# Performance work log

Measured on AMD Instinct MI355X. Metric: run time of the kernel, lower is better.

## Reference

```python
import jax, jax.numpy as jnp
import numpy as np
import math

MIN_NORM = 1e-15
EPS = 1e-7
MAX_NORM = 1e6

N = 100000      # num nodes (aaa)
E = 1600000     # num edges
D_IN = 129      # embedding_num (1 time coord + 128 spatial)
D_OUT = 128     # output1_dim
MAXLEN = 50
B = 4096
NCLASS = 5

# ---------------- Hyperboloid manifold ops (HGCN-style) ----------------

def proj(x, c):
    K = 1. / c
    y = x[..., 1:]
    y_sq = jnp.sum(y * y, axis=-1, keepdims=True)
    x0 = jnp.sqrt(jnp.clip(K + y_sq, EPS))
    return jnp.concatenate([x0, y], axis=-1)

def proj_tan0(u, c):
    # zero out the time coordinate
    return jnp.concatenate([jnp.zeros_like(u[..., :1]), u[..., 1:]], axis=-1)

def expmap0(u, c):
    K = 1. / c
    sqrtK = jnp.sqrt(K)
    x = u[..., 1:]
    xn = jnp.maximum(jnp.linalg.norm(x, axis=-1, keepdims=True), MIN_NORM)
    theta = xn / sqrtK
    first = sqrtK * jnp.cosh(theta)
    rest = sqrtK * jnp.sinh(theta) * x / xn
    return proj(jnp.concatenate([first, rest], axis=-1), c)

def logmap0(x, c):
    K = 1. / c
    sqrtK = jnp.sqrt(K)
    y = x[..., 1:]
    yn = jnp.maximum(jnp.linalg.norm(y, axis=-1, keepdims=True), MIN_NORM)
    theta = jnp.clip(x[..., 0:1] / sqrtK, 1.0 + EPS)
    rest = sqrtK * jnp.arccosh(theta) * y / yn
    return jnp.concatenate([jnp.zeros_like(theta), rest], axis=-1)

def minkowski_dot(x, y):
    return jnp.sum(x * y, axis=-1, keepdims=True) - 2.0 * x[..., 0:1] * y[..., 0:1]

def minkowski_norm(u):
    return jnp.sqrt(jnp.clip(minkowski_dot(u, u), EPS))

def expmap(u, x, c):
    K = 1. / c
    sqrtK = jnp.sqrt(K)
    normu = jnp.minimum(minkowski_norm(u), MAX_NORM)
    theta = jnp.maximum(normu / sqrtK, MIN_NORM)
    result = jnp.cosh(theta) * x + jnp.sinh(theta) * u / theta
    return proj(result, c)

def proj_tan(u, x, c):
    ux = jnp.sum(x[..., 1:] * u[..., 1:], axis=-1, keepdims=True)
    vals0 = ux / jnp.clip(x[..., 0:1], EPS)
    return jnp.concatenate([vals0, u[..., 1:]], axis=-1)

def ptransp0(x, u, c):
    K = 1. / c
    sqrtK = jnp.sqrt(K)
    x0 = x[..., 0:1]
    y = x[..., 1:]
    yn = jnp.maximum(jnp.linalg.norm(y, axis=-1, keepdims=True), MIN_NORM)
    yhat = y / yn
    v = jnp.concatenate([-yn, (sqrtK - x0) * yhat], axis=-1)
    alpha = jnp.sum(yhat * u[..., 1:], axis=-1, keepdims=True) / sqrtK
    return proj_tan(u - alpha * v, x, c)

def mobius_add(x, y, c):
    u = logmap0(y, c)
    v = ptransp0(x, jnp.broadcast_to(u, x.shape), c)
    return expmap(v, x, c)

def mobius_add0(x, y, c):
    # tangent-space addition at the origin
    return expmap0(logmap0(x, c) + logmap0(y, c), c)

def mobius_matvec1(m, x, c):
    return expmap0(logmap0(x, c) @ m, c)

def mobius_matvec0(n, x, c):
    # per-row scalar mobius scaling (n is (N,1))
    return expmap0(n * logmap0(x, c), c)

def hyp_bias_point(b, c):
    return proj(expmap0(proj_tan0(b[None, :], c), c), c)

def gcn_layer(x, w, b, rows, cols, vals, c, n_nodes):
    out = mobius_matvec1(w, x, c)
    out = mobius_add(out, hyp_bias_point(b, c), c)
    out = logmap0(out, c)
    out = jax.ops.segment_sum(vals[:, None] * out[cols], rows, num_segments=n_nodes)
    return proj(expmap0(out, c), c)


def setup_inputs() -> dict:
    key = jax.random.key(0)
    ks = jax.random.split(key, 20)
    def ku(k, shape, fan_in):
        bound = 1.0 / math.sqrt(fan_in)
        return jax.random.uniform(k, shape, jnp.float32, -bound, bound)
    inp = {}
    inp['A1_tensor'] = jax.random.normal(ks[0], (N, D_IN), jnp.float32)
    inp['adj_rows'] = jax.random.randint(ks[1], (E,), 0, N)
    inp['adj_cols'] = jax.random.randint(ks[2], (E,), 0, N)
    inp['adj_vals'] = jax.random.uniform(ks[3], (E,), jnp.float32) * 0.1
    inp['batch_idx'] = jax.random.randint(ks[4], (B, 1, MAXLEN), 0, N)
    inp['raw_c'] = jnp.array([math.log(math.exp(1.0) - 1.0)], jnp.float32)
    inp['n_param'] = jax.random.uniform(ks[5], (N, 1), jnp.float32)
    inp['Lin1'] = ku(ks[6], (D_IN, D_OUT), D_IN)
    inp['Lin1_bias'] = ku(ks[7], (D_OUT,), D_IN)
    inp['gc1_w'] = ku(ks[8], (D_IN, D_OUT), D_IN)
    inp['gc1_b'] = ku(ks[9], (D_OUT,), D_IN)
    inp['gc2_w'] = ku(ks[10], (D_OUT, D_OUT), D_OUT)
    inp['gc2_b'] = ku(ks[11], (D_OUT,), D_OUT)
    inp['weight'] = ku(ks[12], (D_OUT, MAXLEN), D_OUT)
    inp['weight2'] = ku(ks[13], (D_OUT, MAXLEN), D_OUT)
    inp['conv1_w'] = ku(ks[14], (MAXLEN,), MAXLEN)
    inp['conv1_b'] = ku(ks[15], (1,), MAXLEN)
    inp['conv2_w'] = ku(ks[16], (MAXLEN,), MAXLEN)
    inp['conv2_b'] = ku(ks[17], (1,), MAXLEN)
    inp['classifier'] = ku(ks[18], (2 * MAXLEN, NCLASS), 2 * MAXLEN)
    inp['classifier_bias'] = ku(ks[19], (NCLASS,), 2 * MAXLEN)
    return inp


def reference(A1_tensor, adj_rows, adj_cols, adj_vals, batch_idx, raw_c, n_param,
              Lin1, Lin1_bias, gc1_w, gc1_b, gc2_w, gc2_b, weight, weight2,
              conv1_w, conv1_b, conv2_w, conv2_b, classifier, classifier_bias):
    c = jax.nn.softplus(raw_c)[0] + 1e-5
    bi = batch_idx[:, 0, :]                       # (B, L)
    flat = bi.reshape(-1)

    x_tan = proj_tan0(A1_tensor, c)
    a = proj(expmap0(x_tan, c), c)                # (N, D_IN)

    a1 = mobius_matvec1(Lin1, a, c)               # (N, D_OUT)
    a1 = mobius_add(a1, hyp_bias_point(Lin1_bias, c), c)
    a2 = mobius_matvec0(n_param, a1, c)

    x_1 = gcn_layer(a, gc1_w, gc1_b, adj_rows, adj_cols, adj_vals, c, N)
    x_1 = mobius_matvec0(1.0 - n_param, x_1, c)
    x_1 = mobius_add0(x_1, a2, c)
    x_2 = gcn_layer(x_1, gc2_w, gc2_b, adj_rows, adj_cols, adj_vals, c, N)

    # readout branch 1: x_2 gathered on batch indices
    s2 = logmap0(x_2[flat].reshape(bi.shape[0], bi.shape[1], D_OUT), c)  # (B,L,D)
    s2 = jnp.einsum('bld,dt->blt', s2, weight)    # (B, L, MAXLEN)
    s2 = jnp.einsum('blt,l->bt', s2, conv1_w) + conv1_b  # kernel-size-1 conv over channels

    # readout branch 2: a1 gathered on batch indices
    s3 = logmap0(a1[flat].reshape(bi.shape[0], bi.shape[1], D_OUT), c)
    s3 = jnp.einsum('bld,dt->blt', s3, weight2)
    s3 = jnp.einsum('blt,l->bt', s3, conv2_w) + conv2_b

    sel = jnp.concatenate([s2, s3], axis=1)       # (B, 2*MAXLEN)
    pre = sel @ classifier + classifier_bias      # (B, NCLASS)
    return jnp.argmax(pre, axis=-1), sel
```

## Files before the change

### kernel.cpp

```cpp
#include <hip/hip_runtime.h>
#include <math.h>


typedef unsigned short ushort_t;
typedef __attribute__((ext_vector_type(8))) short short8;
typedef __attribute__((ext_vector_type(4))) float f32x4;

__device__ __forceinline__ float wsum(float x){
  x += __shfl_xor(x, 32);
  x += __shfl_xor(x, 16);
  x += __shfl_xor(x, 8);
  x += __shfl_xor(x, 4);
  x += __shfl_xor(x, 2);
  x += __shfl_xor(x, 1);
  return x;
}

__device__ __forceinline__ void get_c(const float* rc, float& K, float& sK){
  float c = log1pf(expf(rc[0])) + 1e-5f;
  K  = 1.0f / c;
  sK = sqrtf(K);
}

__device__ __forceinline__ float sinhx_over_x(float x){
  if (x > 1e-3f){
    float e  = __expf(x);
    float em = __builtin_amdgcn_rcpf(e);
    return 0.5f*(e - em) * __builtin_amdgcn_rcpf(x);
  }
  return 1.0f + x*x*(1.0f/6.0f);
}

__device__ __forceinline__ float facosh(float x){
  return __logf(x + sqrtf(fmaxf(fmaf(x, x, -1.0f), 0.0f)));
}

__device__ __forceinline__ ushort_t bf16_rne(float x){
  unsigned int u = __float_as_uint(x);
  u += 0x7fffu + ((u >> 16) & 1u);
  return (ushort_t)(u >> 16);
}
__device__ __forceinline__ float bf2f(ushort_t h){
  return __uint_as_float(((unsigned int)h) << 16);
}
__device__ __forceinline__ unsigned int pack_bf16(float x, float y){
  unsigned int bx = __float_as_uint(x);
  unsigned int by = __float_as_uint(y);
  bx = (bx + 0x7fffu + ((bx >> 16) & 1u)) >> 16;
  by = (by + 0x7fffu + ((by >> 16) & 1u)) & 0xffff0000u;
  return bx | by;
}
__device__ __forceinline__ float bf_lo(unsigned int p){ return __uint_as_float(p << 16); }
__device__ __forceinline__ float bf_hi(unsigned int p){ return __uint_as_float(p & 0xffff0000u); }

__device__ __forceinline__ void chain_scalars(float tt, float tu, float uu,
                                              float K, float sK,
                                              float& At, float& Au){
  float xn  = fmaxf(sqrtf(tt), 1e-15f);
  float th  = xn / sK;
  float f   = sinhx_over_x(th);
  float pn2 = f*f*tt;
  float p0  = sqrtf(fmaxf(K + pn2, 1e-7f));
  float S_yu = f * tu;
  float yn  = fmaxf(sqrtf(pn2), 1e-15f);
  float inv_yn = __builtin_amdgcn_rcpf(yn);
  float alpha = S_yu * inv_yn / sK;
  float coef  = alpha * (sK - p0);
  float cy  = coef * inv_yn;
  float cyf = cy * f;
  float pdw  = S_yu - cy*pn2;
  float spsq = uu - 2.f*cy*S_yu + cy*cy*pn2;
  float w0 = pdw / fmaxf(p0, 1e-7f);
  float md = spsq - w0*w0;
  float normu = fminf(sqrtf(fmaxf(md, 1e-7f)), 1e6f);
  float th2 = fmaxf(normu / sK, 1e-15f);
  float e  = __expf(th2);
  float em = __builtin_amdgcn_rcpf(e);
  float ch = 0.5f*(e + em);
  float g  = (th2 > 1e-3f) ? 0.5f*(e - em)*__builtin_amdgcn_rcpf(th2)
                           : 1.0f + th2*th2*(1.0f/6.0f);
  float rn2 = ch*ch*pn2 + 2.f*ch*g*pdw + g*g*spsq;
  float r0 = sqrtf(fmaxf(K + rn2, 1e-7f));
  float ynf = fmaxf(sqrtf(rn2), 1e-15f);
  float thf = fmaxf(r0/sK, 1.f+1e-7f);
  float rf = sK * facosh(thf) * __builtin_amdgcn_rcpf(ynf);
  At = rf*(ch*f - g*cyf);
  Au = rf*g;
}

__global__ __launch_bounds__(256) void stage_a(const float* __restrict__ A1,
                                               ushort_t* __restrict__ Lhi,
                                               ushort_t* __restrict__ Llo,
                                               int* __restrict__ cnt,
                                               const float* __restrict__ b0,
                                               const float* __restrict__ b1,
                                               const float* __restrict__ b2,
                                               float* __restrict__ uu3, int n){
  size_t i = (size_t)blockIdx.x * 256 + threadIdx.x;
  size_t total = (size_t)n * 128;
  if (i < total){
    size_t row = i >> 7; int j = (int)(i & 127);
    float v = A1[row*129 + 1 + j];
    ushort_t h = bf16_rne(v);
    Lhi[i] = h;
    Llo[i] = bf16_rne(v - bf2f(h));
  }
  if (i < (size_t)n) cnt[i] = 0;
  if (blockIdx.x == 0 && threadIdx.x < 64){
    int lane = threadIdx.x;
    const float* bs[3] = {b0, b1, b2};
    for (int k = 0; k < 3; ++k){
      float x = lane ? bs[k][2*lane] : 0.0f;
      float y = bs[k][2*lane+1];
      float s = wsum(x*x + y*y);
      if (lane == 0) uu3[k] = s;
    }
  }
}

__global__ __launch_bounds__(256) void split_w(const float* __restrict__ W,
                                               ushort_t* __restrict__ Whi,
                                               ushort_t* __restrict__ Wlo){
  int id = blockIdx.x * 256 + threadIdx.x;
  int k = id >> 7, nn = id & 127;
  float v = W[(size_t)k*128 + nn];
  ushort_t h = bf16_rne(v);
  Whi[(size_t)nn*128 + k] = h;
  Wlo[(size_t)nn*128 + k] = bf16_rne(v - bf2f(h));
}

__global__ __launch_bounds__(256) void mfma_chain(const ushort_t* __restrict__ Ahi,
                                                  const ushort_t* __restrict__ Alo,
                                                  const ushort_t* __restrict__ Whi,
                                                  const ushort_t* __restrict__ Wlo,
                                                  const float* __restrict__ bias,
                                                  const float* __restrict__ uu3, int uuidx,
                                                  const float* __restrict__ raw_c,
                                                  float* __restrict__ outF,
                                                  unsigned int* __restrict__ outH,
                                                  int mode, int n, int nWaves){
  __shared__ ushort_t Wsh[2][128*128];
  int tid = threadIdx.x;
  {
    const uint4* gh = (const uint4*)Whi;
    const uint4* gl = (const uint4*)Wlo;
    uint4* sh = (uint4*)Wsh[0];
    uint4* sl = (uint4*)Wsh[1];
    #pragma unroll
    for (int i = 0; i < 8; ++i){ sh[tid + 256*i] = gh[tid + 256*i]; }
    #pragma unroll
    for (int i = 0; i < 8; ++i){ sl[tid + 256*i] = gl[tid + 256*i]; }
  }
  __syncthreads();

  int lane = tid & 63;
  int c = lane & 15, quad = lane >> 4;
  int wid = blockIdx.x * 4 + (tid >> 6);
  int nStrips = (n + 15) >> 4;

  float K, sK; get_c(raw_c, K, sK);
  float uu = uu3[uuidx];
  float uv[8];
  #pragma unroll
  for (int t = 0; t < 8; ++t){
    int col = t*16 + c;
    uv[t] = (col == 0) ? 0.f : bias[col];
  }

  for (int strip = wid; strip < nStrips; strip += nWaves){
    int m0 = strip * 16;
    int ra = m0 + c; if (ra > n - 1) ra = n - 1;
    short8 ahi[4], alo[4];
    #pragma unroll
    for (int kc = 0; kc < 4; ++kc){
      size_t aoff = (size_t)ra*128 + kc*32 + quad*8;
      ahi[kc] = *(const short8*)&Ahi[aoff];
      alo[kc] = *(const short8*)&Alo[aoff];
    }

    f32x4 acc[8];
    #pragma unroll
    for (int t = 0; t < 8; ++t){
      f32x4 z = {0.f, 0.f, 0.f, 0.f};
      acc[t] = z;
      int wrow = (t*16 + c) * 128;
      #pragma unroll
      for (int kc = 0; kc < 4; ++kc){
        int woff = wrow + kc*32 + quad*8;
        short8 bhi = *(const short8*)&Wsh[0][woff];
        short8 blo = *(const short8*)&Wsh[1][woff];
        acc[t] = __builtin_amdgcn_mfma_f32_16x16x32_bf16(ahi[kc], bhi, acc[t], 0, 0, 0);
        acc[t] = __builtin_amdgcn_mfma_f32_16x16x32_bf16(ahi[kc], blo, acc[t], 0, 0, 0);
        acc[t] = __builtin_amdgcn_mfma_f32_16x16x32_bf16(alo[kc], bhi, acc[t], 0, 0, 0);
      }
    }

    if (c == 0){
      f32x4 z = {0.f, 0.f, 0.f, 0.f};
      acc[0] = z;
    }
    #pragma unroll
    for (int r = 0; r < 4; ++r){
      float tt = 0.f, tu = 0.f;
      #pragma unroll
      for (int t = 0; t < 8; ++t){
        float v = acc[t][r];
        tt = fmaf(v, v, tt);
        tu = fmaf(v, uv[t], tu);
      }
      #pragma unroll
      for (int m = 1; m <= 8; m <<= 1){
        tt += __shfl_xor(tt, m);
        tu += __shfl_xor(tu, m);
      }
      float At, Au; chain_scalars(tt, tu, uu, K, sK, At, Au);
      int row = m0 + quad*4 + r;
      if (mode == 0){
        if (row < n){
          #pragma unroll
          for (int t = 0; t < 8; ++t){
            float o = fmaf(At, acc[t][r], Au*uv[t]);
            outF[(size_t)row*128 + t*16 + c] = o;
          }
        }
      } else {
        #pragma unroll
        for (int t = 0; t < 8; ++t){
          float o  = fmaf(At, acc[t][r], Au*uv[t]);
          float on = __shfl_xor(o, 1);
          if (row < n && !(c & 1))
            outH[(size_t)row*64 + t*8 + (c >> 1)] = pack_bf16(o, on);
        }
      }
    }
  }
}

__global__ __launch_bounds__(256) void hist_k(const int* __restrict__ rows,
                                              int* __restrict__ cnt,
                                              int* __restrict__ rnk, int e){
  int base = (blockIdx.x * 256 + threadIdx.x) * 4;
  if (base + 3 < e){
    int4 r = *(const int4*)&rows[base];
    int k0 = atomicAdd(&cnt[r.x], 1);
    int k1 = atomicAdd(&cnt[r.y], 1);
    int k2 = atomicAdd(&cnt[r.z], 1);
    int k3 = atomicAdd(&cnt[r.w], 1);
    *(int4*)&rnk[base] = make_int4(k0, k1, k2, k3);
  } else {
    for (int i = base; i < e; ++i) rnk[i] = atomicAdd(&cnt[rows[i]], 1);
  }
}

#define SCAN_ITEMS 4
__global__ __launch_bounds__(256) void scan1(const int* __restrict__ cnt,
                                             int* __restrict__ off,
                                             int* __restrict__ bsum, int n){
  __shared__ int sh[256];
  int tid = threadIdx.x;
  int base = blockIdx.x * 256 * SCAN_ITEMS + tid * SCAN_ITEMS;
  int v[SCAN_ITEMS]; int s = 0;
  #pragma unroll
  for (int i = 0; i < SCAN_ITEMS; ++i){ int idx = base+i; v[i] = (idx < n) ? cnt[idx] : 0; s += v[i]; }
  sh[tid] = s; __syncthreads();
  for (int o = 1; o < 256; o <<= 1){
    int t = (tid >= o) ? sh[tid - o] : 0; __syncthreads();
    sh[tid] += t; __syncthreads();
  }
  int excl = sh[tid] - s;
  if (tid == 255) bsum[blockIdx.x] = sh[tid];
  int run = excl;
  #pragma unroll
  for (int i = 0; i < SCAN_ITEMS; ++i){ int idx = base+i; if (idx < n) off[idx] = run; run += v[i]; }
}

__global__ void scan2(int* bsum, int G){
  if (threadIdx.x == 0 && blockIdx.x == 0){
    int run = 0;
    for (int i = 0; i < G; ++i){ int t = bsum[i]; bsum[i] = run; run += t; }
  }
}

__global__ void scan3(int* __restrict__ off, const int* __restrict__ bsum, int n){
  int i = blockIdx.x * blockDim.x + threadIdx.x;
  if (i < n) off[i] += bsum[i / (256*SCAN_ITEMS)];
}

__global__ __launch_bounds__(256) void fill_k(const int* __restrict__ rows,
                                              const int* __restrict__ cols,
                                              const float* __restrict__ vals,
                                              const int* __restrict__ off,
                                              const int* __restrict__ rnk,
                                              int2* __restrict__ ecv, int e){
  int base = (blockIdx.x * 256 + threadIdx.x) * 4;
  if (base + 3 < e){
    int4   r = *(const int4*)&rows[base];
    int4   q = *(const int4*)&rnk[base];
    int4   c = *(const int4*)&cols[base];
    float4 v = *(const float4*)&vals[base];
    int o0 = off[r.x], o1 = off[r.y], o2 = off[r.z], o3 = off[r.w];
    ecv[o0 + q.x] = make_int2(c.x, __float_as_int(v.x));
    ecv[o1 + q.y] = make_int2(c.y, __float_as_int(v.y));
    ecv[o2 + q.z] = make_int2(c.z, __float_as_int(v.z));
    ecv[o3 + q.w] = make_int2(c.w, __float_as_int(v.w));
  } else {
    for (int i = base; i < e; ++i)
      ecv[off[rows[i]] + rnk[i]] = make_int2(cols[i], __float_as_int(vals[i]));
  }
}

__device__ __forceinline__ float2 seg_gather_bf16(const unsigned int* __restrict__ h,
                                                  const int* __restrict__ off,
                                                  const int* __restrict__ cnt,
                                                  const int2* __restrict__ ecv,
                                                  int row, int lane){
  float ax = 0.f, ay = 0.f, bx = 0.f, by = 0.f;
  int st = off[row], deg = cnt[row];
  const unsigned int* __restrict__ hb = h + lane;
  for (int b = 0; b < deg; b += 64){
    int k = b + lane;
    int cc = 0; float vv = 0.f;
    if (k < deg){ int2 e = ecv[st+k]; cc = e.x; vv = __int_as_float(e.y); }
    int m = min(64, deg - b);
    for (int j = 0; j < m; j += 8){
      int   c0=__shfl(cc,j+0), c1=__shfl(cc,j+1), c2=__shfl(cc,j+2), c3=__shfl(cc,j+3);
      int   c4=__shfl(cc,j+4), c5=__shfl(cc,j+5), c6=__shfl(cc,j+6), c7=__shfl(cc,j+7);
      float v0=__shfl(vv,j+0), v1=__shfl(vv,j+1), v2=__shfl(vv,j+2), v3=__shfl(vv,j+3);
      float v4=__shfl(vv,j+4), v5=__shfl(vv,j+5), v6=__shfl(vv,j+6), v7=__shfl(vv,j+7);
      unsigned int p0 = hb[(size_t)c0*64];
      unsigned int p1 = hb[(size_t)c1*64];
      unsigned int p2 = hb[(size_t)c2*64];
      unsigned int p3 = hb[(size_t)c3*64];
      unsigned int p4 = hb[(size_t)c4*64];
      unsigned int p5 = hb[(size_t)c5*64];
      unsigned int p6 = hb[(size_t)c6*64];
      unsigned int p7 = hb[(size_t)c7*64];
      ax = fmaf(v0, bf_lo(p0), ax); ay = fmaf(v0, bf_hi(p0), ay);
      bx = fmaf(v1, bf_lo(p1), bx); by = fmaf(v1, bf_hi(p1), by);
      ax = fmaf(v2, bf_lo(p2), ax); ay = fmaf(v2, bf_hi(p2), ay);
      bx = fmaf(v3, bf_lo(p3), bx); by = fmaf(v3, bf_hi(p3), by);
      ax = fmaf(v4, bf_lo(p4), ax); ay = fmaf(v4, bf_hi(p4), ay);
      bx = fmaf(v5, bf_lo(p5), bx); by = fmaf(v5, bf_hi(p5), by);
      ax = fmaf(v6, bf_lo(p6), ax); ay = fmaf(v6, bf_hi(p6), ay);
      bx = fmaf(v7, bf_lo(p7), bx); by = fmaf(v7, bf_hi(p7), by);
    }
  }
  return make_float2(ax + bx, ay + by);
}

__global__ __launch_bounds__(256) void seg_x1(const unsigned int* __restrict__ h1,
                                              const int* __restrict__ off,
                                              const int* __restrict__ cnt,
                                              const int2* __restrict__ ecv,
                                              const float* __restrict__ loga1,
                                              const float* __restrict__ nparam,
                                              unsigned int* __restrict__ X1hi,
                                              unsigned int* __restrict__ X1lo, int n){
  int row  = (int)((blockIdx.x * blockDim.x + threadIdx.x) >> 6);
  int lane = threadIdx.x & 63;
  if (row >= n) return;
  float2 acc = seg_gather_bf16(h1, off, cnt, ecv, row, lane);
  float nv = nparam[row];
  float2 la1 = *(const float2*)&loga1[(size_t)row*128 + 2*lane];
  float ox = (1.f-nv)*acc.x + nv*la1.x;
  float oy = (1.f-nv)*acc.y + nv*la1.y;
  unsigned int hp = pack_bf16(ox, oy);
  X1hi[(size_t)row*64 + lane] = hp;
  X1lo[(size_t)row*64 + lane] = pack_bf16(ox - bf_lo(hp), oy - bf_hi(hp));
}

__global__ __launch_bounds__(256) void seg_x2(const unsigned int* __restrict__ h2,
                                              const int* __restrict__ off,
                                              const int* __restrict__ cnt,
                                              const int2* __restrict__ ecv,
                                              float* __restrict__ Lx2, int n){
  int row  = (int)((blockIdx.x * blockDim.x + threadIdx.x) >> 6);
  int lane = threadIdx.x & 63;
  if (row >= n) return;
  float2 acc = seg_gather_bf16(h2, off, cnt, ecv, row, lane);
  *(float2*)&Lx2[(size_t)row*128 + 2*lane] = acc;
}

__global__ __launch_bounds__(128) void batch_head(const float* __restrict__ Lx2,
                                                  const float* __restrict__ loga1,
                                                  const int* __restrict__ bidx,
                                                  const float* __restrict__ weight,
                                                  const float* __restrict__ weight2,
                                                  const float* __restrict__ c1w,
                                                  const float* __restrict__ c1b,
                                                  const float* __restrict__ c2w,
                                                  const float* __restrict__ c2b,
                                                  const float* __restrict__ cls,
                                                  const float* __restrict__ clsb,
                                                  float* __restrict__ out, int Bn){
  __shared__ float sg2[128], sg3[128], ssel[100], spre[5];
  __shared__ int sbi[50];
  __shared__ float sc1[50], sc2[50];
  int b = blockIdx.x, d = threadIdx.x;
  const int* bi = bidx + (size_t)b * 50;
  if (d < 50){ sbi[d] = bi[d]; sc1[d] = c1w[d]; sc2[d] = c2w[d]; }
  __syncthreads();
  int lane = d & 63;
  bool lo = d < 64;
  const float* __restrict__ tab = lo ? Lx2 : loga1;
  const float* __restrict__ cw = lo ? sc1 : sc2;
  float gx = 0.f, gy = 0.f;
  const float2* __restrict__ t2 = (const float2*)tab + lane;
  #pragma unroll
  for (int l = 0; l < 50; l += 5){
    int i0 = sbi[l+0], i1 = sbi[l+1], i2 = sbi[l+2], i3 = sbi[l+3], i4 = sbi[l+4];
    float2 p0 = t2[(size_t)i0*64];
    float2 p1 = t2[(size_t)i1*64];
    float2 p2 = t2[(size_t)i2*64];
    float2 p3 = t2[(size_t)i3*64];
    float2 p4 = t2[(size_t)i4*64];
    float w0 = cw[l+0], w1 = cw[l+1], w2 = cw[l+2], w3 = cw[l+3], w4 = cw[l+4];
    gx = fmaf(w0, p0.x, gx); gy = fmaf(w0, p0.y, gy);
    gx = fmaf(w1, p1.x, gx); gy = fmaf(w1, p1.y, gy);
    gx = fmaf(w2, p2.x, gx); gy = fmaf(w2, p2.y, gy);
    gx = fmaf(w3, p3.x, gx); gy = fmaf(w3, p3.y, gy);
    gx = fmaf(w4, p4.x, gx); gy = fmaf(w4, p4.y, gy);
  }
  if (lo){ sg2[2*lane] = gx; sg2[2*lane+1] = gy; }
  else   { sg3[2*lane] = gx; sg3[2*lane+1] = gy; }
  __syncthreads();
  if (d < 50){
    float s = 0.f;
    for (int k = 0; k < 128; ++k) s = fmaf(sg2[k], weight[k*50 + d], s);
    s += c1b[0];
    ssel[d] = s;
    out[(size_t)Bn + (size_t)b*100 + d] = s;
  } else if (d >= 64 && d < 114){
    int t = d - 64;
    float s = 0.f;
    for (int k = 0; k < 128; ++k) s = fmaf(sg3[k], weight2[k*50 + t], s);
    s += c2b[0];
    ssel[50 + t] = s;
    out[(size_t)Bn + (size_t)b*100 + 50 + t] = s;
  }
  __syncthreads();
  if (d < 5){
    float s = clsb[d];
    for (int j = 0; j < 100; ++j) s = fmaf(ssel[j], cls[j*5 + d], s);
    spre[d] = s;
  }
  __syncthreads();
  if (d == 0){
    int best = 0; float bv = spre[0];
    #pragma unroll
    for (int k = 1; k < 5; ++k) if (spre[k] > bv){ bv = spre[k]; best = k; }
    out[b] = (float)best;
  }
}

extern "C" void kernel_launch(void* const* d_in, const int* in_sizes, int n_in,
                              void* d_out, int out_size, void* d_ws, size_t ws_size,
                              hipStream_t stream) {
  const float* A1     = (const float*)d_in[0];
  const int*   rows   = (const int*)  d_in[1];
  const int*   cols   = (const int*)  d_in[2];
  const float* vals   = (const float*)d_in[3];
  const int*   bidx   = (const int*)  d_in[4];
  const float* raw_c  = (const float*)d_in[5];
  const float* nparam = (const float*)d_in[6];
  const float* Lin1   = (const float*)d_in[7];
  const float* Lin1_b = (const float*)d_in[8];
  const float* gc1_w  = (const float*)d_in[9];
  const float* gc1_b  = (const float*)d_in[10];
  const float* gc2_w  = (const float*)d_in[11];
  const float* gc2_b  = (const float*)d_in[12];
  const float* weight = (const float*)d_in[13];
  const float* weight2= (const float*)d_in[14];
  const float* c1w    = (const float*)d_in[15];
  const float* c1b    = (const float*)d_in[16];
  const float* c2w    = (const float*)d_in[17];
  const float* c2b    = (const float*)d_in[18];
  const float* cls    = (const float*)d_in[19];
  const float* clsb   = (const float*)d_in[20];

  int N  = in_sizes[0] / 129;
  int E  = in_sizes[1];
  int Bn = in_sizes[4] / 50;
  size_t NF = (size_t)N * 128;

  ushort_t* Lhi = (ushort_t*)d_ws;
  ushort_t* Llo = Lhi + NF;
  float*    S0  = (float*)d_ws;
  float*    S3  = (float*)(Llo + NF);
  unsigned int* Hb   = (unsigned int*)(S3 + NF);
  unsigned int* X1hi = Hb + NF/2;
  unsigned int* X1lo = X1hi + NF/2;
  ushort_t* Wb = (ushort_t*)(X1lo + NF/2);
  ushort_t* W1h = Wb,           *W1l = Wb + 16384;
  ushort_t* W2h = Wb + 2*16384, *W2l = Wb + 3*16384;
  ushort_t* W3h = Wb + 4*16384, *W3l = Wb + 5*16384;
  int* cnt    = (int*)(Wb + 6*16384);
  int* off    = cnt + N;
  int* rnk    = off + N;
  int* bsum   = rnk + E;
  int2* ecv   = (int2*)(bsum + 4096);
  float* uu3  = (float*)(ecv + E);

  int rowBlocks  = (N + 3) / 4;
  int G = (N + 256*SCAN_ITEMS - 1) / (256*SCAN_ITEMS);
  int eBlocks4 = (E/4 + 255) / 256 + 1;
  int mBlocks = 512;
  int nWaves  = mBlocks * 4;

  stage_a<<<(int)((NF + 255)/256), 256, 0, stream>>>(A1, Lhi, Llo, cnt,
                                                     Lin1_b, gc1_b, gc2_b, uu3, N);
  split_w<<<64, 256, 0, stream>>>(Lin1 + 128, W1h, W1l);
  split_w<<<64, 256, 0, stream>>>(gc1_w + 128, W2h, W2l);
  split_w<<<64, 256, 0, stream>>>(gc2_w, W3h, W3l);

  hist_k<<<eBlocks4, 256, 0, stream>>>(rows, cnt, rnk, E);
  scan1<<<G, 256, 0, stream>>>(cnt, off, bsum, N);
  scan2<<<1, 64, 0, stream>>>(bsum, G);
  scan3<<<(N+255)/256, 256, 0, stream>>>(off, bsum, N);
  fill_k<<<eBlocks4, 256, 0, stream>>>(rows, cols, vals, off, rnk, ecv, E);

  mfma_chain<<<mBlocks, 256, 0, stream>>>(Lhi, Llo, W1h, W1l, Lin1_b, uu3, 0, raw_c,
                                          S3, (unsigned int*)nullptr, 0, N, nWaves);
  mfma_chain<<<mBlocks, 256, 0, stream>>>(Lhi, Llo, W2h, W2l, gc1_b, uu3, 1, raw_c,
                                          (float*)nullptr, Hb, 1, N, nWaves);
  seg_x1<<<rowBlocks, 256, 0, stream>>>(Hb, off, cnt, ecv, S3, nparam, X1hi, X1lo, N);
  mfma_chain<<<mBlocks, 256, 0, stream>>>((const ushort_t*)X1hi, (const ushort_t*)X1lo,
                                          W3h, W3l, gc2_b, uu3, 2, raw_c,
                                          (float*)nullptr, Hb, 1, N, nWaves);
  seg_x2<<<rowBlocks, 256, 0, stream>>>(Hb, off, cnt, ecv, S0, N);
  batch_head<<<Bn, 128, 0, stream>>>(S0, S3, bidx, weight, weight2, c1w, c1b,
                                     c2w, c2b, cls, clsb, (float*)d_out, Bn);
}
```

Before: 625.5 us.

## Overlap CSR build and readout branch with MFMA GEMMs via auxiliary warps

The edge histogram, CSR fill, and the a1 readout branch move into extra warps of the mfma_chain launches, so this latency-bound scatter and gather work overlaps the GEMM passes. Those launches grow from 256 to 320 or 384 threads. The change also vectorizes stage_a, merges the three split_w launches into one, parallelizes scan2, and stores the second GCN output as bf16 so the final head gathers half the bytes. The risks are extra register and scheduling pressure on the GEMM blocks, and a small loss of precision in the x_2 readout.

```diff
diff --git a/kernel.cpp b/kernel.cpp
--- a/kernel.cpp
+++ b/kernel.cpp
@@ -5,6 +5,7 @@
 typedef unsigned short ushort_t;
 typedef __attribute__((ext_vector_type(8))) short short8;
 typedef __attribute__((ext_vector_type(4))) float f32x4;
+typedef __attribute__((ext_vector_type(4))) unsigned short u16x4;
 
 __device__ __forceinline__ float wsum(float x){
   x += __shfl_xor(x, 32);
@@ -96,16 +97,20 @@
                                                const float* __restrict__ b1,
                                                const float* __restrict__ b2,
                                                float* __restrict__ uu3, int n){
-  size_t i = (size_t)blockIdx.x * 256 + threadIdx.x;
-  size_t total = (size_t)n * 128;
-  if (i < total){
-    size_t row = i >> 7; int j = (int)(i & 127);
-    float v = A1[row*129 + 1 + j];
-    ushort_t h = bf16_rne(v);
-    Lhi[i] = h;
-    Llo[i] = bf16_rne(v - bf2f(h));
-  }
-  if (i < (size_t)n) cnt[i] = 0;
+  size_t i4 = (size_t)blockIdx.x * 256 + threadIdx.x;
+  size_t tot4 = (size_t)n * 32;
+  if (i4 < tot4){
+    size_t row = i4 >> 5; int j0 = (int)(i4 & 31) * 4;
+    const float* s = A1 + row*129 + 1 + j0;
+    float v0 = s[0], v1 = s[1], v2 = s[2], v3 = s[3];
+    ushort_t h0 = bf16_rne(v0), h1 = bf16_rne(v1), h2 = bf16_rne(v2), h3 = bf16_rne(v3);
+    u16x4 hh = {h0, h1, h2, h3};
+    u16x4 ll = {bf16_rne(v0 - bf2f(h0)), bf16_rne(v1 - bf2f(h1)),
+                bf16_rne(v2 - bf2f(h2)), bf16_rne(v3 - bf2f(h3))};
+    *(u16x4*)&Lhi[i4*4] = hh;
+    *(u16x4*)&Llo[i4*4] = ll;
+  }
+  if (i4 < (size_t)n) cnt[i4] = 0;
   if (blockIdx.x == 0 && threadIdx.x < 64){
     int lane = threadIdx.x;
     const float* bs[3] = {b0, b1, b2};
@@ -118,10 +123,16 @@
   }
 }
 
-__global__ __launch_bounds__(256) void split_w(const float* __restrict__ W,
-                                               ushort_t* __restrict__ Whi,
-                                               ushort_t* __restrict__ Wlo){
-  int id = blockIdx.x * 256 + threadIdx.x;
+__global__ __launch_bounds__(256) void split_w3(const float* __restrict__ Lin1,
+                                                const float* __restrict__ G1,
+                                                const float* __restrict__ G2,
+                                                ushort_t* __restrict__ Wb){
+  int bid = blockIdx.x;
+  int which = bid >> 6, b = bid & 63;
+  const float* W = (which == 0) ? (Lin1 + 128) : (which == 1) ? (G1 + 128) : G2;
+  ushort_t* Whi = Wb + (size_t)which * 2 * 16384;
+  ushort_t* Wlo = Whi + 16384;
+  int id = b * 256 + threadIdx.x;
   int k = id >> 7, nn = id & 127;
   float v = W[(size_t)k*128 + nn];
   ushort_t h = bf16_rne(v);
@@ -129,7 +140,7 @@
   Wlo[(size_t)nn*128 + k] = bf16_rne(v - bf2f(h));
 }
 
-__global__ __launch_bounds__(256) void mfma_chain(const ushort_t* __restrict__ Ahi,
+__global__ __launch_bounds__(384) void mfma_chain(const ushort_t* __restrict__ Ahi,
                                                   const ushort_t* __restrict__ Alo,
                                                   const ushort_t* __restrict__ Whi,
                                                   const ushort_t* __restrict__ Wlo,
@@ -138,10 +149,25 @@
                                                   const float* __restrict__ raw_c,
                                                   float* __restrict__ outF,
                                                   unsigned int* __restrict__ outH,
-                                                  int mode, int n, int nWaves){
+                                                  int mode, int n, int nWaves,
+                                                  int aux, int epb, int e,
+                                                  const int* __restrict__ erows,
+                                                  const int* __restrict__ ecols,
+                                                  const float* __restrict__ evals,
+                                                  int* __restrict__ cnt,
+                                                  int* __restrict__ rnk,
+                                                  const int* __restrict__ off,
+                                                  int2* __restrict__ ecv,
+                                                  const float* __restrict__ loga1,
+                                                  const int* __restrict__ bidx,
+                                                  const float* __restrict__ c2w,
+                                                  const float* __restrict__ c2b,
+                                                  const float* __restrict__ weight2,
+                                                  float* __restrict__ sel3,
+                                                  float* __restrict__ outTop, int Bn){
   __shared__ ushort_t Wsh[2][128*128];
   int tid = threadIdx.x;
-  {
+  if (tid < 256){
     const uint4* gh = (const uint4*)Whi;
     const uint4* gl = (const uint4*)Wlo;
     uint4* sh = (uint4*)Wsh[0];
@@ -154,8 +180,91 @@
   __syncthreads();
 
   int lane = tid & 63;
+  int warp = tid >> 6;
+
+  if (warp >= 4){
+    if (aux == 1){
+      int gpl = epb >> 8;
+      int gbase = (blockIdx.x * epb) >> 2;
+      for (int k = 0; k < gpl; ++k){
+        int b4 = (gbase + k*64 + lane) * 4;
+        if (b4 + 3 < e){
+          int4 r = *(const int4*)&erows[b4];
+          int k0 = atomicAdd(&cnt[r.x], 1);
+          int k1 = atomicAdd(&cnt[r.y], 1);
+          int k2 = atomicAdd(&cnt[r.z], 1);
+          int k3 = atomicAdd(&cnt[r.w], 1);
+          *(int4*)&rnk[b4] = make_int4(k0, k1, k2, k3);
+        } else {
+          for (int i = b4; i < e; ++i) rnk[i] = atomicAdd(&cnt[erows[i]], 1);
+        }
+      }
+    } else if (aux == 2){
+      int gpl = epb >> 8;
+      int gbase = (blockIdx.x * epb) >> 2;
+      for (int k = 0; k < gpl; ++k){
+        int b4 = (gbase + k*64 + lane) * 4;
+        if (b4 + 3 < e){
+          int4   r = *(const int4*)&erows[b4];
+          int4   q = *(const int4*)&rnk[b4];
+          int4   cc = *(const int4*)&ecols[b4];
+          float4 vv = *(const float4*)&evals[b4];
+          int o0 = off[r.x], o1 = off[r.y], o2 = off[r.z], o3 = off[r.w];
+          ecv[o0 + q.x] = make_int2(cc.x, __float_as_int(vv.x));
+          ecv[o1 + q.y] = make_int2(cc.y, __float_as_int(vv.y));
+          ecv[o2 + q.z] = make_int2(cc.z, __float_as_int(vv.z));
+          ecv[o3 + q.w] = make_int2(cc.w, __float_as_int(vv.w));
+        } else {
+          for (int i = b4; i < e; ++i)
+            ecv[off[erows[i]] + rnk[i]] = make_int2(ecols[i], __float_as_int(evals[i]));
+        }
+      }
+    } else if (aux == 3){
+      float cw = (lane < 50) ? c2w[lane] : 0.f;
+      for (int q = 0; q < 4; ++q){
+        int b = blockIdx.x * 8 + (warp - 4) * 4 + q;
+        if (b >= Bn) break;
+        int bi = (lane < 50) ? bidx[(size_t)b*50 + lane] : 0;
+        float gx = 0.f, gy = 0.f;
+        #pragma unroll
+        for (int l = 0; l < 50; l += 5){
+          int i0 = __shfl(bi, l+0), i1 = __shfl(bi, l+1), i2 = __shfl(bi, l+2);
+          int i3 = __shfl(bi, l+3), i4 = __shfl(bi, l+4);
+          float w0 = __shfl(cw, l+0), w1 = __shfl(cw, l+1), w2v = __shfl(cw, l+2);
+          float w3 = __shfl(cw, l+3), w4 = __shfl(cw, l+4);
+          float2 p0 = *(const float2*)&loga1[(size_t)i0*128 + 2*lane];
+          float2 p1 = *(const float2*)&loga1[(size_t)i1*128 + 2*lane];
+          float2 p2 = *(const float2*)&loga1[(size_t)i2*128 + 2*lane];
+          float2 p3 = *(const float2*)&loga1[(size_t)i3*128 + 2*lane];
+          float2 p4 = *(const float2*)&loga1[(size_t)i4*128 + 2*lane];
+          gx = fmaf(w0, p0.x, gx); gy = fmaf(w0, p0.y, gy);
+          gx = fmaf(w1, p1.x, gx); gy = fmaf(w1, p1.y, gy);
+          gx = fmaf(w2v, p2.x, gx); gy = fmaf(w2v, p2.y, gy);
+          gx = fmaf(w3, p3.x, gx); gy = fmaf(w3, p3.y, gy);
+          gx = fmaf(w4, p4.x, gx); gy = fmaf(w4, p4.y, gy);
+        }
+        float s = 0.f;
+        #pragma unroll 8
+        for (int d = 0; d < 128; d += 2){
+          float ge = __shfl(gx, d >> 1);
+          float go = __shfl(gy, d >> 1);
+          if (lane < 50){
+            s = fmaf(ge, weight2[d*50 + lane], s);
+            s = fmaf(go, weight2[(d+1)*50 + lane], s);
+          }
+        }
+        if (lane < 50){
+          float v = s + c2b[0];
+          sel3[(size_t)b*50 + lane] = v;
+          outTop[(size_t)Bn + (size_t)b*100 + 50 + lane] = v;
+        }
+      }
+    }
+    return;
+  }
+
   int c = lane & 15, quad = lane >> 4;
-  int wid = blockIdx.x * 4 + (tid >> 6);
+  int wid = blockIdx.x * 4 + warp;
   int nStrips = (n + 15) >> 4;
 
   float K, sK; get_c(raw_c, K, sK);
@@ -236,22 +345,6 @@
   }
 }
 
-__global__ __launch_bounds__(256) void hist_k(const int* __restrict__ rows,
-                                              int* __restrict__ cnt,
-                                              int* __restrict__ rnk, int e){
-  int base = (blockIdx.x * 256 + threadIdx.x) * 4;
-  if (base + 3 < e){
-    int4 r = *(const int4*)&rows[base];
-    int k0 = atomicAdd(&cnt[r.x], 1);
-    int k1 = atomicAdd(&cnt[r.y], 1);
-    int k2 = atomicAdd(&cnt[r.z], 1);
-    int k3 = atomicAdd(&cnt[r.w], 1);
-    *(int4*)&rnk[base] = make_int4(k0, k1, k2, k3);
-  } else {
-    for (int i = base; i < e; ++i) rnk[i] = atomicAdd(&cnt[rows[i]], 1);
-  }
-}
-
 #define SCAN_ITEMS 4
 __global__ __launch_bounds__(256) void scan1(const int* __restrict__ cnt,
                                              int* __restrict__ off,
@@ -274,39 +367,21 @@
   for (int i = 0; i < SCAN_ITEMS; ++i){ int idx = base+i; if (idx < n) off[idx] = run; run += v[i]; }
 }
 
-__global__ void scan2(int* bsum, int G){
-  if (threadIdx.x == 0 && blockIdx.x == 0){
-    int run = 0;
-    for (int i = 0; i < G; ++i){ int t = bsum[i]; bsum[i] = run; run += t; }
-  }
+__global__ __launch_bounds__(256) void scan2(int* __restrict__ bsum, int G){
+  __shared__ int sh[256];
+  int t = threadIdx.x;
+  int v = (t < G) ? bsum[t] : 0;
+  sh[t] = v; __syncthreads();
+  for (int o = 1; o < 256; o <<= 1){
+    int x = (t >= o) ? sh[t - o] : 0; __syncthreads();
+    sh[t] += x; __syncthreads();
+  }
+  if (t < G) bsum[t] = sh[t] - v;
 }
 
 __global__ void scan3(int* __restrict__ off, const int* __restrict__ bsum, int n){
   int i = blockIdx.x * blockDim.x + threadIdx.x;
   if (i < n) off[i] += bsum[i / (256*SCAN_ITEMS)];
-}
-
-__global__ __launch_bounds__(256) void fill_k(const int* __restrict__ rows,
-                                              const int* __restrict__ cols,
-                                              const float* __restrict__ vals,
-                                              const int* __restrict__ off,
-                                              const int* __restrict__ rnk,
-                                              int2* __restrict__ ecv, int e){
-  int base = (blockIdx.x * 256 + threadIdx.x) * 4;
-  if (base + 3 < e){
-    int4   r = *(const int4*)&rows[base];
-    int4   q = *(const int4*)&rnk[base];
-    int4   c = *(const int4*)&cols[base];
-    float4 v = *(const float4*)&vals[base];
-    int o0 = off[r.x], o1 = off[r.y], o2 = off[r.z], o3 = off[r.w];
-    ecv[o0 + q.x] = make_int2(c.x, __float_as_int(v.x));
-    ecv[o1 + q.y] = make_int2(c.y, __float_as_int(v.y));
-    ecv[o2 + q.z] = make_int2(c.z, __float_as_int(v.z));
-    ecv[o3 + q.w] = make_int2(c.w, __float_as_int(v.w));
-  } else {
-    for (int i = base; i < e; ++i)
-      ecv[off[rows[i]] + rnk[i]] = make_int2(cols[i], __float_as_int(vals[i]));
-  }
 }
 
 __device__ __forceinline__ float2 seg_gather_bf16(const unsigned int* __restrict__ h,
@@ -373,79 +448,71 @@
                                               const int* __restrict__ off,
                                               const int* __restrict__ cnt,
                                               const int2* __restrict__ ecv,
-                                              float* __restrict__ Lx2, int n){
+                                              unsigned int* __restrict__ Lx2p, int n){
   int row  = (int)((blockIdx.x * blockDim.x + threadIdx.x) >> 6);
   int lane = threadIdx.x & 63;
   if (row >= n) return;
   float2 acc = seg_gather_bf16(h2, off, cnt, ecv, row, lane);
-  *(float2*)&Lx2[(size_t)row*128 + 2*lane] = acc;
-}
-
-__global__ __launch_bounds__(128) void batch_head(const float* __restrict__ Lx2,
-                                                  const float* __restrict__ loga1,
-                                                  const int* __restrict__ bidx,
-                                                  const float* __restrict__ weight,
-                                                  const float* __restrict__ weight2,
-                                                  const float* __restrict__ c1w,
-                                                  const float* __restrict__ c1b,
-                                                  const float* __restrict__ c2w,
-                                                  const float* __restrict__ c2b,
-                                                  const float* __restrict__ cls,
-                                                  const float* __restrict__ clsb,
-                                                  float* __restrict__ out, int Bn){
-  __shared__ float sg2[128], sg3[128], ssel[100], spre[5];
-  __shared__ int sbi[50];
-  __shared__ float sc1[50], sc2[50];
-  int b = blockIdx.x, d = threadIdx.x;
-  const int* bi = bidx + (size_t)b * 50;
-  if (d < 50){ sbi[d] = bi[d]; sc1[d] = c1w[d]; sc2[d] = c2w[d]; }
-  __syncthreads();
-  int lane = d & 63;
-  bool lo = d < 64;
-  const float* __restrict__ tab = lo ? Lx2 : loga1;
-  const float* __restrict__ cw = lo ? sc1 : sc2;
+  Lx2p[(size_t)row*64 + lane] = pack_bf16(acc.x, acc.y);
+}
+
+__global__ __launch_bounds__(64) void head_s2(const unsigned int* __restrict__ Lx2p,
+                                              const float* __restrict__ sel3,
+                                              const int* __restrict__ bidx,
+                                              const float* __restrict__ weight,
+                                              const float* __restrict__ c1w,
+                                              const float* __restrict__ c1b,
+                                              const float* __restrict__ cls,
+                                              const float* __restrict__ clsb,
+                                              float* __restrict__ out, int Bn){
+  __shared__ float ssel[100];
+  __shared__ float spre[5];
+  int b = blockIdx.x, lane = threadIdx.x;
+  float cw = (lane < 50) ? c1w[lane] : 0.f;
+  int bi  = (lane < 50) ? bidx[(size_t)b*50 + lane] : 0;
   float gx = 0.f, gy = 0.f;
-  const float2* __restrict__ t2 = (const float2*)tab + lane;
+  const unsigned int* __restrict__ tp = Lx2p + lane;
   #pragma unroll
   for (int l = 0; l < 50; l += 5){
-    int i0 = sbi[l+0], i1 = sbi[l+1], i2 = sbi[l+2], i3 = sbi[l+3], i4 = sbi[l+4];
-    float2 p0 = t2[(size_t)i0*64];
-    float2 p1 = t2[(size_t)i1*64];
-    float2 p2 = t2[(size_t)i2*64];
-    float2 p3 = t2[(size_t)i3*64];
-    float2 p4 = t2[(size_t)i4*64];
-    float w0 = cw[l+0], w1 = cw[l+1], w2 = cw[l+2], w3 = cw[l+3], w4 = cw[l+4];
-    gx = fmaf(w0, p0.x, gx); gy = fmaf(w0, p0.y, gy);
-    gx = fmaf(w1, p1.x, gx); gy = fmaf(w1, p1.y, gy);
-    gx = fmaf(w2, p2.x, gx); gy = fmaf(w2, p2.y, gy);
-    gx = fmaf(w3, p3.x, gx); gy = fmaf(w3, p3.y, gy);
-    gx = fmaf(w4, p4.x, gx); gy = fmaf(w4, p4.y, gy);
-  }
-  if (lo){ sg2[2*lane] = gx; sg2[2*lane+1] = gy; }
-  else   { sg3[2*lane] = gx; sg3[2*lane+1] = gy; }
+    int i0 = __shfl(bi, l+0), i1 = __shfl(bi, l+1), i2 = __shfl(bi, l+2);
+    int i3 = __shfl(bi, l+3), i4 = __shfl(bi, l+4);
+    float w0 = __shfl(cw, l+0), w1 = __shfl(cw, l+1), w2v = __shfl(cw, l+2);
+    float w3 = __shfl(cw, l+3), w4 = __shfl(cw, l+4);
+    unsigned int p0 = tp[(size_t)i0*64];
+    unsigned int p1 = tp[(size_t)i1*64];
+    unsigned int p2 = tp[(size_t)i2*64];
+    unsigned int p3 = tp[(size_t)i3*64];
+    unsigned int p4 = tp[(size_t)i4*64];
+    gx = fmaf(w0, bf_lo(p0), gx); gy = fmaf(w0, bf_hi(p0), gy);
+    gx = fmaf(w1, bf_lo(p1), gx); gy = fmaf(w1, bf_hi(p1), gy);
+    gx = fmaf(w2v, bf_lo(p2), gx); gy = fmaf(w2v, bf_hi(p2), gy);
+    gx = fmaf(w3, bf_lo(p3), gx); gy = fmaf(w3, bf_hi(p3), gy);
+    gx = fmaf(w4, bf_lo(p4), gx); gy = fmaf(w4, bf_hi(p4), gy);
+  }
+  float s = 0.f;
+  #pragma unroll 8
+  for (int d = 0; d < 128; d += 2){
+    float ge = __shfl(gx, d >> 1);
+    float go = __shfl(gy, d >> 1);
+    if (lane < 50){
+      s = fmaf(ge, weight[d*50 + lane], s);
+      s = fmaf(go, weight[(d+1)*50 + lane], s);
+    }
+  }
+  if (lane < 50){
+    float v = s + c1b[0];
+    ssel[lane] = v;
+    out[(size_t)Bn + (size_t)b*100 + lane] = v;
+    ssel[50 + lane] = sel3[(size_t)b*50 + lane];
+  }
   __syncthreads();
-  if (d < 50){
-    float s = 0.f;
-    for (int k = 0; k < 128; ++k) s = fmaf(sg2[k], weight[k*50 + d], s);
-    s += c1b[0];
-    ssel[d] = s;
-    out[(size_t)Bn + (size_t)b*100 + d] = s;
-  } else if (d >= 64 && d < 114){
-    int t = d - 64;
-    float s = 0.f;
-    for (int k = 0; k < 128; ++k) s = fmaf(sg3[k], weight2[k*50 + t], s);
-    s += c2b[0];
-    ssel[50 + t] = s;
-    out[(size_t)Bn + (size_t)b*100 + 50 + t] = s;
+  if (lane < 5){
+    float sc = clsb[lane];
+    for (int j = 0; j < 100; ++j) sc = fmaf(ssel[j], cls[j*5 + lane], sc);
+    spre[lane] = sc;
   }
   __syncthreads();
-  if (d < 5){
-    float s = clsb[d];
-    for (int j = 0; j < 100; ++j) s = fmaf(ssel[j], cls[j*5 + d], s);
-    spre[d] = s;
-  }
-  __syncthreads();
-  if (d == 0){
+  if (lane == 0){
     int best = 0; float bv = spre[0];
     #pragma unroll
     for (int k = 1; k < 5; ++k) if (spre[k] > bv){ bv = spre[k]; best = k; }
@@ -485,7 +552,7 @@
 
   ushort_t* Lhi = (ushort_t*)d_ws;
   ushort_t* Llo = Lhi + NF;
-  float*    S0  = (float*)d_ws;
+  unsigned int* Lx2p = (unsigned int*)d_ws;
   float*    S3  = (float*)(Llo + NF);
   unsigned int* Hb   = (unsigned int*)(S3 + NF);
   unsigned int* X1hi = Hb + NF/2;
@@ -500,34 +567,42 @@
   int* bsum   = rnk + E;
   int2* ecv   = (int2*)(bsum + 4096);
   float* uu3  = (float*)(ecv + E);
+  float* sel3 = (float*)rnk;
 
   int rowBlocks  = (N + 3) / 4;
   int G = (N + 256*SCAN_ITEMS - 1) / (256*SCAN_ITEMS);
-  int eBlocks4 = (E/4 + 255) / 256 + 1;
   int mBlocks = 512;
   int nWaves  = mBlocks * 4;
-
-  stage_a<<<(int)((NF + 255)/256), 256, 0, stream>>>(A1, Lhi, Llo, cnt,
-                                                     Lin1_b, gc1_b, gc2_b, uu3, N);
-  split_w<<<64, 256, 0, stream>>>(Lin1 + 128, W1h, W1l);
-  split_w<<<64, 256, 0, stream>>>(gc1_w + 128, W2h, W2l);
-  split_w<<<64, 256, 0, stream>>>(gc2_w, W3h, W3l);
-
-  hist_k<<<eBlocks4, 256, 0, stream>>>(rows, cnt, rnk, E);
+  int epb = (((E + mBlocks - 1) / mBlocks) + 255) & ~255;
+
+  stage_a<<<(int)((N*32 + 255)/256), 256, 0, stream>>>(A1, Lhi, Llo, cnt,
+                                                       Lin1_b, gc1_b, gc2_b, uu3, N);
+  split_w3<<<192, 256, 0, stream>>>(Lin1, gc1_w, gc2_w, Wb);
+
+  mfma_chain<<<mBlocks, 320, 0, stream>>>(Lhi, Llo, W1h, W1l, Lin1_b, uu3, 0, raw_c,
+                                          S3, (unsigned int*)nullptr, 0, N, nWaves,
+                                          1, epb, E, rows, cols, vals, cnt, rnk, off, ecv,
+                                          nullptr, nullptr, nullptr, nullptr, nullptr,
+                                          nullptr, nullptr, 0);
   scan1<<<G, 256, 0, stream>>>(cnt, off, bsum, N);
-  scan2<<<1, 64, 0, stream>>>(bsum, G);
+  scan2<<<1, 256, 0, stream>>>(bsum, G);
   scan3<<<(N+255)/256, 256, 0, stream>>>(off, bsum, N);
-  fill_k<<<eBlocks4, 256, 0, stream>>>(rows, cols, vals, off, rnk, ecv, E);
-
-  mfma_chain<<<mBlocks, 256, 0, stream>>>(Lhi, Llo, W1h, W1l, Lin1_b, uu3, 0, raw_c,
-                                          S3, (unsigned int*)nullptr, 0, N, nWaves);
-  mfma_chain<<<mBlocks, 256, 0, stream>>>(Lhi, Llo, W2h, W2l, gc1_b, uu3, 1, raw_c,
-                                          (float*)nullptr, Hb, 1, N, nWaves);
+
+  mfma_chain<<<mBlocks, 320, 0, stream>>>(Lhi, Llo, W2h, W2l, gc1_b, uu3, 1, raw_c,
+                                          (float*)nullptr, Hb, 1, N, nWaves,
+                                          2, epb, E, rows, cols, vals, cnt, rnk, off, ecv,
+                                          nullptr, nullptr, nullptr, nullptr, nullptr,
+                                          nullptr, nullptr, 0);
   seg_x1<<<rowBlocks, 256, 0, stream>>>(Hb, off, cnt, ecv, S3, nparam, X1hi, X1lo, N);
-  mfma_chain<<<mBlocks, 256, 0, stream>>>((const ushort_t*)X1hi, (const ushort_t*)X1lo,
+
+  mfma_chain<<<mBlocks, 384, 0, stream>>>((const ushort_t*)X1hi, (const ushort_t*)X1lo,
                                           W3h, W3l, gc2_b, uu3, 2, raw_c,
-                                          (float*)nullptr, Hb, 1, N, nWaves);
-  seg_x2<<<rowBlocks, 256, 0, stream>>>(Hb, off, cnt, ecv, S0, N);
-  batch_head<<<Bn, 128, 0, stream>>>(S0, S3, bidx, weight, weight2, c1w, c1b,
-                                     c2w, c2b, cls, clsb, (float*)d_out, Bn);
-}
+                                          (float*)nullptr, Hb, 1, N, nWaves,
+                                          3, 0, 0, nullptr, nullptr, nullptr,
+                                          nullptr, nullptr, nullptr, nullptr,
+                                          S3, bidx, c2w, c2b, weight2, sel3,
+                                          (float*)d_out, Bn);
+  seg_x2<<<rowBlocks, 256, 0, stream>>>(Hb, off, cnt, ecv, Lx2p, N);
+  head_s2<<<Bn, 64, 0, stream>>>(Lx2p, sel3, bidx, weight, c1w, c1b,
+                                 cls, clsb, (float*)d_out, Bn);
+}
```

After: 699.2 us. +11.8%, slower.
